# Performance work log

Hardware: AMD Instinct MI355X
Metric: run time of the kernel (lower is better)

The kernel has to match this reference:

```python
import jax, jax.numpy as jnp
import numpy as np

N, E, D = 50000, 800000, 128  # nodes, edges, n_feat


def setup_inputs() -> dict:
    key = jax.random.key(0)
    ks = jax.random.split(key, 12)
    scale = 1.0 / np.sqrt(D)

    def w(k):
        return jax.random.normal(k, (D, D), jnp.float32) * scale

    return {
        "h": jax.random.normal(ks[0], (N, D), jnp.float32),
        "src": jax.random.randint(ks[1], (E,), 0, N, jnp.int32),
        "dst": jax.random.randint(ks[2], (E,), 0, N, jnp.int32),
        # skip MLP: Linear -> ELU -> Linear
        "W_skip1": w(ks[3]), "b_skip1": jnp.zeros((D,), jnp.float32),
        "W_skip2": w(ks[4]), "b_skip2": jnp.zeros((D,), jnp.float32),
        # SAGEConv 1 (mean aggregator): fc_self, fc_neigh (bias-free) + shared bias
        "W_self1": w(ks[5]), "W_neigh1": w(ks[6]), "b_conv1": jnp.zeros((D,), jnp.float32),
        # self-interaction MLP
        "W_si1": w(ks[7]), "b_si1": jnp.zeros((D,), jnp.float32),
        "W_si2": w(ks[8]), "b_si2": jnp.zeros((D,), jnp.float32),
        # SAGEConv 2
        "W_self2": w(ks[9]), "W_neigh2": w(ks[10]), "b_conv2": jnp.zeros((D,), jnp.float32),
    }


def _sage_mean(h, src, dst, W_self, W_neigh, b):
    # DGL SAGEConv('mean'): fc_self(h) + fc_neigh(mean over in-neighbors of h_src) + bias
    n = h.shape[0]
    deg = jax.ops.segment_sum(jnp.ones((src.shape[0],), h.dtype), dst, num_segments=n)
    agg = jax.ops.segment_sum(h[src], dst, num_segments=n)  # [N, D] sum of neighbor feats
    agg = agg / jnp.maximum(deg, 1.0)[:, None]  # degree clamp for isolated nodes
    return h @ W_self + agg @ W_neigh + b


def reference(h, src, dst,
              W_skip1, b_skip1, W_skip2, b_skip2,
              W_self1, W_neigh1, b_conv1,
              W_si1, b_si1, W_si2, b_si2,
              W_self2, W_neigh2, b_conv2):
    elu = jax.nn.elu
    h_skip = elu(h @ W_skip1 + b_skip1) @ W_skip2 + b_skip2
    x = elu(_sage_mean(h, src, dst, W_self1, W_neigh1, b_conv1))
    x = elu(elu(x @ W_si1 + b_si1) @ W_si2 + b_si2)
    x = _sage_mean(x, src, dst, W_self2, W_neigh2, b_conv2)
    return h_skip + x
```

## Files before the change

kernel.cpp:

```cpp
#include <hip/hip_runtime.h>
#include <math.h>

#define NN 50000
#define NE 800000
#define NRT 782
#define NT  (NRT * 2)
#define NB  128
#define NPB2 391
#define EPB 2048
#define NBB 391

typedef __attribute__((ext_vector_type(8))) short short8;
typedef __attribute__((ext_vector_type(4))) float floatx4;

#define AS1 __attribute__((address_space(1)))
#define AS3 __attribute__((address_space(3)))

__device__ __forceinline__ unsigned short f2bf(float f) {
    unsigned u = __float_as_uint(f);
    unsigned r = (u + 0x7fff + ((u >> 16) & 1)) >> 16;
    return (unsigned short)r;
}
__device__ __forceinline__ float bf2f(unsigned short h) {
    return __uint_as_float(((unsigned)h) << 16);
}


__global__ __launch_bounds__(256)
void k_prep(const float* __restrict__ h, unsigned short* __restrict__ hB,
            const int* __restrict__ dst, int* __restrict__ bcnt,
            const float* w0, const float* w1, const float* w2, const float* w3,
            const float* w4, const float* w5, const float* w6, const float* w7,
            short* __restrict__ wpk) {
    int bid = blockIdx.x;
    const int t = threadIdx.x;
    if (bid < 3125) {
        int i = (bid * 256 + t) * 8;
        float4 a = *(const float4*)&h[i];
        float4 b = *(const float4*)&h[i + 4];
        short8 v;
        v[0] = (short)f2bf(a.x); v[1] = (short)f2bf(a.y);
        v[2] = (short)f2bf(a.z); v[3] = (short)f2bf(a.w);
        v[4] = (short)f2bf(b.x); v[5] = (short)f2bf(b.y);
        v[6] = (short)f2bf(b.z); v[7] = (short)f2bf(b.w);
        *(short8*)&hB[i] = v;
    } else if (bid < 3125 + NBB) {
        __shared__ int cnt[NB];
        if (t < NB) cnt[t] = 0;
        __syncthreads();
        int base = (bid - 3125) * EPB;
#pragma unroll
        for (int i = 0; i < 8; ++i) {
            int idx = base + i * 256 + t;
            if (idx < NE) atomicAdd(&cnt[dst[idx] / NPB2], 1);
        }
        __syncthreads();
        if (t < NB && cnt[t]) atomicAdd(&bcnt[t], cnt[t]);
    } else {
        int wb = bid - 3125 - NBB;
        const float* W;
        switch (wb) {
            case 0: W = w0; break; case 1: W = w1; break;
            case 2: W = w2; break; case 3: W = w3; break;
            case 4: W = w4; break; case 5: W = w5; break;
            case 6: W = w6; break; default: W = w7; break;
        }
        short* dstp = wpk + (size_t)wb * 16384;
#pragma unroll
        for (int i = 0; i < 8; ++i) {
            int q = t + i * 256;
            int cb = q >> 8, ks = (q >> 6) & 3, lane = q & 63;
            int n = lane & 15, g = lane >> 4;
            int col = cb * 16 + n, krow = ks * 32 + g * 8;
            short8 v;
#pragma unroll
            for (int j = 0; j < 8; ++j)
                v[j] = (short)f2bf(W[(krow + j) * 128 + col]);
            *(short8*)&dstp[q * 8] = v;
        }
    }
}


__global__ void k_bscan(const int* __restrict__ bcnt, int* __restrict__ gcur,
                        int* __restrict__ bstart) {
    __shared__ int s[NB];
    int t = threadIdx.x;
    int c = bcnt[t];
    s[t] = c;
    __syncthreads();
    for (int off = 1; off < NB; off <<= 1) {
        int v = (t >= off) ? s[t - off] : 0;
        __syncthreads();
        s[t] += v;
        __syncthreads();
    }
    int excl = s[t] - c;
    gcur[t] = excl;
    bstart[t] = excl;
    if (t == NB - 1) bstart[NB] = s[NB - 1];
}


__global__ __launch_bounds__(256)
void k_bucket(const int* __restrict__ src, const int* __restrict__ dst,
              int* __restrict__ gcur, int* __restrict__ bsrc, int* __restrict__ bdst) {
    __shared__ int psrc[EPB];
    __shared__ int pdst[EPB];
    __shared__ int cnt[NB];
    __shared__ int ebase[NB];
    __shared__ int gbase[NB];
    const int t = threadIdx.x;
    const int e0 = blockIdx.x * EPB;
    const int M = (e0 + EPB <= NE) ? EPB : (NE - e0);

    if (t < NB) cnt[t] = 0;
    __syncthreads();

    int es[8], ed[8], rank[8];
#pragma unroll
    for (int i = 0; i < 8; ++i) {
        int idx = i * 256 + t;
        if (idx < M) {
            es[i] = src[e0 + idx];
            ed[i] = dst[e0 + idx];
            rank[i] = atomicAdd(&cnt[ed[i] / NPB2], 1);
        }
    }
    __syncthreads();
    if (t < NB) ebase[t] = cnt[t];
    __syncthreads();
    for (int off = 1; off < NB; off <<= 1) {
        int v = 0;
        if (t < NB && t >= off) v = ebase[t - off];
        __syncthreads();
        if (t < NB) ebase[t] += v;
        __syncthreads();
    }
    if (t < NB) ebase[t] -= cnt[t];
    __syncthreads();
#pragma unroll
    for (int i = 0; i < 8; ++i) {
        int idx = i * 256 + t;
        if (idx < M) {
            int b = ed[i] / NPB2;
            int pos = ebase[b] + rank[i];
            psrc[pos] = es[i];
            pdst[pos] = ed[i];
        }
    }
    if (t < NB && cnt[t] > 0) gbase[t] = atomicAdd(&gcur[t], cnt[t]);
    __syncthreads();
#pragma unroll
    for (int i = 0; i < 8; ++i) {
        int idx = i * 256 + t;
        if (idx < M) {
            int d = pdst[idx];
            int b = d / NPB2;
            int gpos = gbase[b] + (idx - ebase[b]);
            bsrc[gpos] = psrc[idx];
            bdst[gpos] = d;
        }
    }
}


template<int DUAL, int DOELU, int OUTF32, int NOBIAS, int BIAS2>
__device__ __forceinline__ void gemm_body(
        int bid,
        const unsigned short* __restrict__ A, const unsigned short* __restrict__ A2,
        const short* __restrict__ Wp, const short* __restrict__ Wp2,
        const float* __restrict__ bias, const float* __restrict__ bias2,
        void* outv, short* sW, short* sA) {
    const int t = threadIdx.x;
    const int wv = t >> 6, lane = t & 63;
    const int rb = bid >> 1, ct = bid & 1;
    const int row0 = rb * 64, col0 = ct * 64;
    const int m = lane & 15, g = lane >> 4;

    floatx4 acc[4];
#pragma unroll
    for (int cb = 0; cb < 4; ++cb) acc[cb] = (floatx4){0.f, 0.f, 0.f, 0.f};

    const int npass = DUAL ? 2 : 1;
    for (int pass = 0; pass < npass; ++pass) {
        const unsigned short* Ac = pass ? A2 : A;
        const short* Wc = (pass ? Wp2 : Wp) + ct * 8192;
        __syncthreads();
#pragma unroll
        for (int i = 0; i < 4; ++i) {
            int cbase = (i * 4 + wv) * 64;
            __builtin_amdgcn_global_load_lds(
                (const AS1 unsigned int*)(Wc + (size_t)(cbase + lane) * 8),
                (AS3 unsigned int*)(sW + cbase * 8), 16, 0, 0);
        }
#pragma unroll
        for (int i = 0; i < 4; ++i) {
            int cbase = (i * 4 + wv) * 64;
            int id = cbase + lane;
            int r = id >> 4, cs = id & 15;
            int rg = row0 + r; if (rg >= NN) rg = NN - 1;
            int csrc = cs ^ (r & 7);
            __builtin_amdgcn_global_load_lds(
                (const AS1 unsigned int*)(Ac + (size_t)rg * 128 + csrc * 8),
                (AS3 unsigned int*)(sA + cbase * 8), 16, 0, 0);
        }
        asm volatile("s_waitcnt vmcnt(0)" ::: "memory");
        __builtin_amdgcn_sched_barrier(0);
        __syncthreads();

        const int r0 = wv * 16;
#pragma unroll
        for (int ks = 0; ks < 4; ++ks) {
            int cxor = (ks * 4 + g) ^ (m & 7);
            short8 af = *(const short8*)&sA[((r0 + m) * 16 + cxor) * 8];
#pragma unroll
            for (int cb = 0; cb < 4; ++cb) {
                short8 bf = *(const short8*)&sW[((cb * 4 + ks) * 64 + lane) * 8];
                acc[cb] = __builtin_amdgcn_mfma_f32_16x16x32_bf16(af, bf, acc[cb], 0, 0, 0);
            }
        }
    }

    const int rowbase = row0 + wv * 16 + g * 4;
#pragma unroll
    for (int cb = 0; cb < 4; ++cb) {
        int C = col0 + cb * 16 + m;
        float bb = NOBIAS ? 0.f : bias[C];
        if (BIAS2) bb += bias2[C];
#pragma unroll
        for (int rr = 0; rr < 4; ++rr) {
            int R = rowbase + rr;
            if (R < NN) {
                size_t idx = (size_t)R * 128 + C;
                float v = acc[cb][rr] + bb;
                if (DOELU) v = (v > 0.f) ? v : expm1f(v);
                if (OUTF32) ((float*)outv)[idx] = v;
                else        ((unsigned short*)outv)[idx] = f2bf(v);
            }
        }
    }
}

template<int DUAL, int DOELU, int OUTF32, int NOBIAS, int BIAS2>
__global__ __launch_bounds__(256)
void k_mm(const unsigned short* __restrict__ A, const unsigned short* __restrict__ A2,
          const short* __restrict__ Wp, const short* __restrict__ Wp2,
          const float* __restrict__ bias, const float* __restrict__ bias2,
          void* outv) {
    __shared__ short sMem[16384];
    gemm_body<DUAL, DOELU, OUTF32, NOBIAS, BIAS2>(blockIdx.x, A, A2, Wp, Wp2,
                                                  bias, bias2, outv, sMem, sMem + 8192);
}


__global__ __launch_bounds__(256)
void k_mega1(const int* __restrict__ bsrc, const int* __restrict__ bdst,
             const int* __restrict__ bstart, int* __restrict__ row_start,
             int* __restrict__ col_idx,
             const unsigned short* __restrict__ hB, const short* __restrict__ wpk,
             const float* __restrict__ bsk1,
             unsigned short* __restrict__ T1out, unsigned short* __restrict__ C1out,
             unsigned short* __restrict__ S1out) {
    __shared__ short sMem[16384];
    int bid = blockIdx.x;
    if (bid < NB) {
        int* lcur = (int*)sMem;
        int* sc   = lcur + NPB2;
        int* rs   = sc + 512;
        const int t = threadIdx.x;
        const int n0 = bid * NPB2;
        const int n1 = (n0 + NPB2 < NN) ? n0 + NPB2 : NN;
        const int nn = n1 - n0;
        const int w0 = bstart[bid], w1 = bstart[bid + 1];
        for (int i = t; i < nn; i += 256) lcur[i] = 0;
        __syncthreads();
        for (int e = w0 + t; e < w1; e += 256)
            atomicAdd(&lcur[bdst[e] - n0], 1);
        __syncthreads();
        int v0 = (t < nn) ? lcur[t] : 0;
        int v1 = (t + 256 < nn) ? lcur[t + 256] : 0;
        sc[t] = v0; sc[t + 256] = v1;
        __syncthreads();
        for (int off = 1; off < 512; off <<= 1) {
            int a0 = (t >= off) ? sc[t - off] : 0;
            int a1 = (t + 256 >= off) ? sc[t + 256 - off] : 0;
            __syncthreads();
            sc[t] += a0; sc[t + 256] += a1;
            __syncthreads();
        }
        for (int i = t; i < nn; i += 256) {
            int r = w0 + sc[i] - lcur[i];
            rs[i] = r;
            row_start[n0 + i] = r;
            lcur[i] = 0;
        }
        if (bid == 0 && t == 0) row_start[NN] = NE;
        __syncthreads();
        for (int e = w0 + t; e < w1; e += 256) {
            int d = bdst[e] - n0;
            int slot = atomicAdd(&lcur[d], 1);
            col_idx[rs[d] + slot] = bsrc[e];
        }
    } else if (bid < NB + NT) {
        gemm_body<0, 0, 0, 1, 0>(bid - NB, hB, nullptr, wpk + 3 * 16384, nullptr,
                                 nullptr, nullptr, T1out, sMem, sMem + 8192);
    } else if (bid < NB + 2 * NT) {
        gemm_body<0, 0, 0, 1, 0>(bid - NB - NT, hB, nullptr, wpk + 2 * 16384, nullptr,
                                 nullptr, nullptr, C1out, sMem, sMem + 8192);
    } else {
        gemm_body<0, 1, 0, 0, 0>(bid - NB - 2 * NT, hB, nullptr, wpk, nullptr,
                                 bsk1, nullptr, S1out, sMem, sMem + 8192);
    }
}


__global__ __launch_bounds__(256)
void k_agg1x(const unsigned short* __restrict__ T1, const int* __restrict__ row_start,
             const int* __restrict__ col_idx, const unsigned short* __restrict__ C1,
             const float* __restrict__ bc, unsigned short* __restrict__ X1out) {
    int node = (blockIdx.x * 256 + threadIdx.x) >> 6;
    int lane = threadIdx.x & 63;
    if (node >= NN) return;
    const int beg = row_start[node], end = row_start[node + 1];
    const size_t lo = (size_t)(lane * 2);
    float sx = 0.f, sy = 0.f;
    int j = beg;
#pragma unroll 1
    for (; j + 8 <= end; j += 8) {
        int s[8];
#pragma unroll
        for (int u = 0; u < 8; ++u) s[u] = col_idx[j + u];
        unsigned v[8];
#pragma unroll
        for (int u = 0; u < 8; ++u)
            v[u] = *(const unsigned*)&T1[(size_t)s[u] * 128 + lo];
#pragma unroll
        for (int u = 0; u < 8; ++u) {
            sx += bf2f((unsigned short)(v[u] & 0xffff));
            sy += bf2f((unsigned short)(v[u] >> 16));
        }
    }
#pragma unroll 1
    for (; j < end; ++j) {
        int s = col_idx[j];
        unsigned v = *(const unsigned*)&T1[(size_t)s * 128 + lo];
        sx += bf2f((unsigned short)(v & 0xffff));
        sy += bf2f((unsigned short)(v >> 16));
    }
    float inv = 1.0f / fmaxf((float)(end - beg), 1.0f);
    unsigned c = *(const unsigned*)&C1[(size_t)node * 128 + lo];
    float x = sx * inv + bf2f((unsigned short)(c & 0xffff)) + bc[lane * 2];
    float y = sy * inv + bf2f((unsigned short)(c >> 16)) + bc[lane * 2 + 1];
    x = (x > 0.f) ? x : expm1f(x);
    y = (y > 0.f) ? y : expm1f(y);
    unsigned o = (unsigned)f2bf(x) | ((unsigned)f2bf(y) << 16);
    *(unsigned*)&X1out[(size_t)node * 128 + lo] = o;
}


__global__ __launch_bounds__(256)
void k_mega3(const unsigned short* __restrict__ X3, const unsigned short* __restrict__ S1,
             const short* __restrict__ wpk, const float* __restrict__ bconv2,
             const float* __restrict__ bsk2, float* __restrict__ outP,
             unsigned short* __restrict__ T2out) {
    __shared__ short sMem[16384];
    int bid = blockIdx.x;
    if (bid < NT) {
        gemm_body<1, 0, 1, 0, 1>(bid, X3, S1, wpk + 6 * 16384, wpk + 1 * 16384,
                                 bconv2, bsk2, outP, sMem, sMem + 8192);
    } else {
        gemm_body<0, 0, 0, 1, 0>(bid - NT, X3, nullptr, wpk + 7 * 16384, nullptr,
                                 nullptr, nullptr, T2out, sMem, sMem + 8192);
    }
}


__global__ __launch_bounds__(256)
void k_aggf(const unsigned short* __restrict__ T2, const int* __restrict__ row_start,
            const int* __restrict__ col_idx, float* __restrict__ out) {
    int node = (blockIdx.x * 256 + threadIdx.x) >> 6;
    int lane = threadIdx.x & 63;
    if (node >= NN) return;
    const int beg = row_start[node], end = row_start[node + 1];
    const size_t lo = (size_t)(lane * 2);
    float sx = 0.f, sy = 0.f;
    int j = beg;
#pragma unroll 1
    for (; j + 8 <= end; j += 8) {
        int s[8];
#pragma unroll
        for (int u = 0; u < 8; ++u) s[u] = col_idx[j + u];
        unsigned v[8];
#pragma unroll
        for (int u = 0; u < 8; ++u)
            v[u] = *(const unsigned*)&T2[(size_t)s[u] * 128 + lo];
#pragma unroll
        for (int u = 0; u < 8; ++u) {
            sx += bf2f((unsigned short)(v[u] & 0xffff));
            sy += bf2f((unsigned short)(v[u] >> 16));
        }
    }
#pragma unroll 1
    for (; j < end; ++j) {
        int s = col_idx[j];
        unsigned v = *(const unsigned*)&T2[(size_t)s * 128 + lo];
        sx += bf2f((unsigned short)(v & 0xffff));
        sy += bf2f((unsigned short)(v >> 16));
    }
    float inv = 1.0f / fmaxf((float)(end - beg), 1.0f);
    float2* op = (float2*)&out[(size_t)node * 128 + lo];
    float2 v = *op;
    v.x += sx * inv;
    v.y += sy * inv;
    *op = v;
}


extern "C" void kernel_launch(void* const* d_in, const int* in_sizes, int n_in,
                              void* d_out, int out_size, void* d_ws, size_t ws_size,
                              hipStream_t stream) {
    const float* h        = (const float*)d_in[0];
    const int*   src      = (const int*)d_in[1];
    const int*   dst      = (const int*)d_in[2];
    const float* W_skip1  = (const float*)d_in[3];
    const float* b_skip1  = (const float*)d_in[4];
    const float* W_skip2  = (const float*)d_in[5];
    const float* b_skip2  = (const float*)d_in[6];
    const float* W_self1  = (const float*)d_in[7];
    const float* W_neigh1 = (const float*)d_in[8];
    const float* b_conv1  = (const float*)d_in[9];
    const float* W_si1    = (const float*)d_in[10];
    const float* b_si1    = (const float*)d_in[11];
    const float* W_si2    = (const float*)d_in[12];
    const float* b_si2    = (const float*)d_in[13];
    const float* W_self2  = (const float*)d_in[14];
    const float* W_neigh2 = (const float*)d_in[15];
    const float* b_conv2  = (const float*)d_in[16];
    float* out = (float*)d_out;

    char* ws = (char*)d_ws;
    int* bcnt      = (int*)ws;
    int* gcur      = bcnt + 128;
    int* bstart    = bcnt + 256;
    int* row_start = bcnt + 100096;
    int* col_idx   = bcnt + 150272;
    short* wpk          = (short*)(ws + 3801088);
    unsigned short* hB  = (unsigned short*)(ws + 4063232);
    unsigned short* B1  = (unsigned short*)(ws + 16863232);
    unsigned short* B2  = (unsigned short*)(ws + 29663232);
    int* bsrc           = (int*)(ws + 42463232);
    int* bdst           = (int*)(ws + 45663232);
    unsigned short* C1s = (unsigned short*)d_out;

    hipMemsetAsync(ws, 0, 128 * sizeof(int), stream);

    k_prep<<<3125 + NBB + 8, 256, 0, stream>>>(h, hB, dst, bcnt,
                                               W_skip1, W_skip2, W_self1, W_neigh1,
                                               W_si1, W_si2, W_self2, W_neigh2, wpk);
    k_bscan<<<1, NB, 0, stream>>>(bcnt, gcur, bstart);

    k_bucket<<<NBB, 256, 0, stream>>>(src, dst, gcur, bsrc, bdst);

    k_mega1<<<NB + 3 * NT, 256, 0, stream>>>(bsrc, bdst, bstart, row_start, col_idx,
                                             hB, wpk, b_skip1, B1, C1s, B2);

    k_agg1x<<<12500, 256, 0, stream>>>(B1, row_start, col_idx, C1s, b_conv1, hB);

    k_mm<0, 1, 0, 0, 0><<<NT, 256, 0, stream>>>(hB, nullptr, wpk + 4 * 16384, nullptr,
                                                b_si1, nullptr, B1);
    k_mm<0, 1, 0, 0, 0><<<NT, 256, 0, stream>>>(B1, nullptr, wpk + 5 * 16384, nullptr,
                                                b_si2, nullptr, hB);

    k_mega3<<<2 * NT, 256, 0, stream>>>(hB, B2, wpk, b_conv2, b_skip2, out, B1);

    k_aggf<<<12500, 256, 0, stream>>>(B1, row_start, col_idx, out);
}
```

Measured before the change: 199.5 us.

## Share A tile across three GEMMs and split gather over half-wavefronts

The three GEMMs in the first mega kernel that all read hB now run in one block, which loads the A tile into LDS once and then cycles through the three weight matrices. This replaces three separate block sets that each reloaded the same A rows. Separately, both aggregation kernels now split each wavefront into two halves that handle alternate edges with 8-byte loads, then combine the halves with a cross-lane shuffle. The gather is meant to keep more distinct rows in flight per instruction, at the cost of fewer blocks in the fused GEMM and one extra reduction step.

Result: faster. 189.2 us (-5.1%).

```diff
diff --git a/kernel.cpp b/kernel.cpp
--- a/kernel.cpp
+++ b/kernel.cpp
@@ -254,6 +254,84 @@
 }
 
 
+__device__ __forceinline__ void gemm3_body(
+        int bid, const unsigned short* __restrict__ A,
+        const short* __restrict__ Wn, const short* __restrict__ Ws,
+        const short* __restrict__ Wk, const float* __restrict__ bsk1,
+        unsigned short* __restrict__ T1, unsigned short* __restrict__ C1,
+        unsigned short* __restrict__ S1, short* sW, short* sA) {
+    const int t = threadIdx.x;
+    const int wv = t >> 6, lane = t & 63;
+    const int rb = bid >> 1, ct = bid & 1;
+    const int row0 = rb * 64, col0 = ct * 64;
+    const int m = lane & 15, g = lane >> 4;
+
+#pragma unroll
+    for (int i = 0; i < 4; ++i) {
+        int cbase = (i * 4 + wv) * 64;
+        int id = cbase + lane;
+        int r = id >> 4, cs = id & 15;
+        int rg = row0 + r; if (rg >= NN) rg = NN - 1;
+        int csrc = cs ^ (r & 7);
+        __builtin_amdgcn_global_load_lds(
+            (const AS1 unsigned int*)(A + (size_t)rg * 128 + csrc * 8),
+            (AS3 unsigned int*)(sA + cbase * 8), 16, 0, 0);
+    }
+
+#pragma unroll
+    for (int ph = 0; ph < 3; ++ph) {
+        if (ph) __syncthreads();
+        const short* Wc = (ph == 0 ? Wn : ph == 1 ? Ws : Wk) + ct * 8192;
+#pragma unroll
+        for (int i = 0; i < 4; ++i) {
+            int cbase = (i * 4 + wv) * 64;
+            __builtin_amdgcn_global_load_lds(
+                (const AS1 unsigned int*)(Wc + (size_t)(cbase + lane) * 8),
+                (AS3 unsigned int*)(sW + cbase * 8), 16, 0, 0);
+        }
+        asm volatile("s_waitcnt vmcnt(0)" ::: "memory");
+        __builtin_amdgcn_sched_barrier(0);
+        __syncthreads();
+
+        floatx4 acc[4];
+#pragma unroll
+        for (int cb = 0; cb < 4; ++cb) acc[cb] = (floatx4){0.f, 0.f, 0.f, 0.f};
+        const int r0 = wv * 16;
+#pragma unroll
+        for (int ks = 0; ks < 4; ++ks) {
+            int cxor = (ks * 4 + g) ^ (m & 7);
+            short8 af = *(const short8*)&sA[((r0 + m) * 16 + cxor) * 8];
+#pragma unroll
+            for (int cb = 0; cb < 4; ++cb) {
+                short8 bf = *(const short8*)&sW[((cb * 4 + ks) * 64 + lane) * 8];
+                acc[cb] = __builtin_amdgcn_mfma_f32_16x16x32_bf16(af, bf, acc[cb], 0, 0, 0);
+            }
+        }
+
+        const int rowbase = row0 + wv * 16 + g * 4;
+#pragma unroll
+        for (int cb = 0; cb < 4; ++cb) {
+            int C = col0 + cb * 16 + m;
+            float bb = (ph == 2) ? bsk1[C] : 0.f;
+#pragma unroll
+            for (int rr = 0; rr < 4; ++rr) {
+                int R = rowbase + rr;
+                if (R < NN) {
+                    size_t idx = (size_t)R * 128 + C;
+                    float v = acc[cb][rr] + bb;
+                    if (ph == 0)      T1[idx] = f2bf(v);
+                    else if (ph == 1) C1[idx] = f2bf(v);
+                    else {
+                        v = (v > 0.f) ? v : expm1f(v);
+                        S1[idx] = f2bf(v);
+                    }
+                }
+            }
+        }
+    }
+}
+
+
 __global__ __launch_bounds__(256)
 void k_mega1(const int* __restrict__ bsrc, const int* __restrict__ bdst,
              const int* __restrict__ bstart, int* __restrict__ row_start,
@@ -302,15 +380,9 @@
             int slot = atomicAdd(&lcur[d], 1);
             col_idx[rs[d] + slot] = bsrc[e];
         }
-    } else if (bid < NB + NT) {
-        gemm_body<0, 0, 0, 1, 0>(bid - NB, hB, nullptr, wpk + 3 * 16384, nullptr,
-                                 nullptr, nullptr, T1out, sMem, sMem + 8192);
-    } else if (bid < NB + 2 * NT) {
-        gemm_body<0, 0, 0, 1, 0>(bid - NB - NT, hB, nullptr, wpk + 2 * 16384, nullptr,
-                                 nullptr, nullptr, C1out, sMem, sMem + 8192);
     } else {
-        gemm_body<0, 1, 0, 0, 0>(bid - NB - 2 * NT, hB, nullptr, wpk, nullptr,
-                                 bsk1, nullptr, S1out, sMem, sMem + 8192);
+        gemm3_body(bid - NB, hB, wpk + 3 * 16384 , wpk + 2 * 16384 ,
+                   wpk , bsk1, T1out, C1out, S1out, sMem, sMem + 8192);
     }
 }
 
@@ -322,40 +394,61 @@
     int node = (blockIdx.x * 256 + threadIdx.x) >> 6;
     int lane = threadIdx.x & 63;
     if (node >= NN) return;
+    const int grp = lane >> 5, gl = lane & 31;
     const int beg = row_start[node], end = row_start[node + 1];
-    const size_t lo = (size_t)(lane * 2);
-    float sx = 0.f, sy = 0.f;
+    const size_t lo = (size_t)(gl * 4);
+    float a0 = 0.f, a1 = 0.f, a2 = 0.f, a3 = 0.f;
     int j = beg;
 #pragma unroll 1
     for (; j + 8 <= end; j += 8) {
-        int s[8];
-#pragma unroll
-        for (int u = 0; u < 8; ++u) s[u] = col_idx[j + u];
-        unsigned v[8];
-#pragma unroll
-        for (int u = 0; u < 8; ++u)
-            v[u] = *(const unsigned*)&T1[(size_t)s[u] * 128 + lo];
-#pragma unroll
-        for (int u = 0; u < 8; ++u) {
-            sx += bf2f((unsigned short)(v[u] & 0xffff));
-            sy += bf2f((unsigned short)(v[u] >> 16));
+        int s[4];
+#pragma unroll
+        for (int u = 0; u < 4; ++u) s[u] = col_idx[j + 2 * u + grp];
+        uint2 v[4];
+#pragma unroll
+        for (int u = 0; u < 4; ++u)
+            v[u] = *(const uint2*)&T1[(size_t)s[u] * 128 + lo];
+#pragma unroll
+        for (int u = 0; u < 4; ++u) {
+            a0 += bf2f((unsigned short)(v[u].x & 0xffff));
+            a1 += bf2f((unsigned short)(v[u].x >> 16));
+            a2 += bf2f((unsigned short)(v[u].y & 0xffff));
+            a3 += bf2f((unsigned short)(v[u].y >> 16));
         }
     }
 #pragma unroll 1
-    for (; j < end; ++j) {
-        int s = col_idx[j];
-        unsigned v = *(const unsigned*)&T1[(size_t)s * 128 + lo];
-        sx += bf2f((unsigned short)(v & 0xffff));
-        sy += bf2f((unsigned short)(v >> 16));
-    }
-    float inv = 1.0f / fmaxf((float)(end - beg), 1.0f);
-    unsigned c = *(const unsigned*)&C1[(size_t)node * 128 + lo];
-    float x = sx * inv + bf2f((unsigned short)(c & 0xffff)) + bc[lane * 2];
-    float y = sy * inv + bf2f((unsigned short)(c >> 16)) + bc[lane * 2 + 1];
-    x = (x > 0.f) ? x : expm1f(x);
-    y = (y > 0.f) ? y : expm1f(y);
-    unsigned o = (unsigned)f2bf(x) | ((unsigned)f2bf(y) << 16);
-    *(unsigned*)&X1out[(size_t)node * 128 + lo] = o;
+    for (; j < end; j += 2) {
+        int e = j + grp;
+        if (e < end) {
+            int s = col_idx[e];
+            uint2 v = *(const uint2*)&T1[(size_t)s * 128 + lo];
+            a0 += bf2f((unsigned short)(v.x & 0xffff));
+            a1 += bf2f((unsigned short)(v.x >> 16));
+            a2 += bf2f((unsigned short)(v.y & 0xffff));
+            a3 += bf2f((unsigned short)(v.y >> 16));
+        }
+    }
+    a0 += __shfl_xor(a0, 32);
+    a1 += __shfl_xor(a1, 32);
+    a2 += __shfl_xor(a2, 32);
+    a3 += __shfl_xor(a3, 32);
+    if (lane < 32) {
+        float inv = 1.0f / fmaxf((float)(end - beg), 1.0f);
+        uint2 c = *(const uint2*)&C1[(size_t)node * 128 + lo];
+        float4 bv = *(const float4*)&bc[lane * 4];
+        float x0 = a0 * inv + bf2f((unsigned short)(c.x & 0xffff)) + bv.x;
+        float x1 = a1 * inv + bf2f((unsigned short)(c.x >> 16)) + bv.y;
+        float x2 = a2 * inv + bf2f((unsigned short)(c.y & 0xffff)) + bv.z;
+        float x3 = a3 * inv + bf2f((unsigned short)(c.y >> 16)) + bv.w;
+        x0 = (x0 > 0.f) ? x0 : expm1f(x0);
+        x1 = (x1 > 0.f) ? x1 : expm1f(x1);
+        x2 = (x2 > 0.f) ? x2 : expm1f(x2);
+        x3 = (x3 > 0.f) ? x3 : expm1f(x3);
+        uint2 o;
+        o.x = (unsigned)f2bf(x0) | ((unsigned)f2bf(x1) << 16);
+        o.y = (unsigned)f2bf(x2) | ((unsigned)f2bf(x3) << 16);
+        *(uint2*)&X1out[(size_t)node * 128 + lo] = o;
+    }
 }
 
 
@@ -382,38 +475,52 @@
     int node = (blockIdx.x * 256 + threadIdx.x) >> 6;
     int lane = threadIdx.x & 63;
     if (node >= NN) return;
+    const int grp = lane >> 5, gl = lane & 31;
     const int beg = row_start[node], end = row_start[node + 1];
-    const size_t lo = (size_t)(lane * 2);
-    float sx = 0.f, sy = 0.f;
+    const size_t lo = (size_t)(gl * 4);
+    float a0 = 0.f, a1 = 0.f, a2 = 0.f, a3 = 0.f;
     int j = beg;
 #pragma unroll 1
     for (; j + 8 <= end; j += 8) {
-        int s[8];
-#pragma unroll
-        for (int u = 0; u < 8; ++u) s[u] = col_idx[j + u];
-        unsigned v[8];
-#pragma unroll
-        for (int u = 0; u < 8; ++u)
-            v[u] = *(const unsigned*)&T2[(size_t)s[u] * 128 + lo];
-#pragma unroll
-        for (int u = 0; u < 8; ++u) {
-            sx += bf2f((unsigned short)(v[u] & 0xffff));
-            sy += bf2f((unsigned short)(v[u] >> 16));
+        int s[4];
+#pragma unroll
+        for (int u = 0; u < 4; ++u) s[u] = col_idx[j + 2 * u + grp];
+        uint2 v[4];
+#pragma unroll
+        for (int u = 0; u < 4; ++u)
+            v[u] = *(const uint2*)&T2[(size_t)s[u] * 128 + lo];
+#pragma unroll
+        for (int u = 0; u < 4; ++u) {
+            a0 += bf2f((unsigned short)(v[u].x & 0xffff));
+            a1 += bf2f((unsigned short)(v[u].x >> 16));
+            a2 += bf2f((unsigned short)(v[u].y & 0xffff));
+            a3 += bf2f((unsigned short)(v[u].y >> 16));
         }
     }
 #pragma unroll 1
-    for (; j < end; ++j) {
-        int s = col_idx[j];
-        unsigned v = *(const unsigned*)&T2[(size_t)s * 128 + lo];
-        sx += bf2f((unsigned short)(v & 0xffff));
-        sy += bf2f((unsigned short)(v >> 16));
-    }
-    float inv = 1.0f / fmaxf((float)(end - beg), 1.0f);
-    float2* op = (float2*)&out[(size_t)node * 128 + lo];
-    float2 v = *op;
-    v.x += sx * inv;
-    v.y += sy * inv;
-    *op = v;
+    for (; j < end; j += 2) {
+        int e = j + grp;
+        if (e < end) {
+            int s = col_idx[e];
+            uint2 v = *(const uint2*)&T2[(size_t)s * 128 + lo];
+            a0 += bf2f((unsigned short)(v.x & 0xffff));
+            a1 += bf2f((unsigned short)(v.x >> 16));
+            a2 += bf2f((unsigned short)(v.y & 0xffff));
+            a3 += bf2f((unsigned short)(v.y >> 16));
+        }
+    }
+    a0 += __shfl_xor(a0, 32);
+    a1 += __shfl_xor(a1, 32);
+    a2 += __shfl_xor(a2, 32);
+    a3 += __shfl_xor(a3, 32);
+    if (lane < 32) {
+        float inv = 1.0f / fmaxf((float)(end - beg), 1.0f);
+        float4* op = (float4*)&out[(size_t)node * 128 + lo];
+        float4 v = *op;
+        v.x += a0 * inv; v.y += a1 * inv;
+        v.z += a2 * inv; v.w += a3 * inv;
+        *op = v;
+    }
 }
 
 
@@ -462,8 +569,8 @@
 
     k_bucket<<<NBB, 256, 0, stream>>>(src, dst, gcur, bsrc, bdst);
 
-    k_mega1<<<NB + 3 * NT, 256, 0, stream>>>(bsrc, bdst, bstart, row_start, col_idx,
-                                             hB, wpk, b_skip1, B1, C1s, B2);
+    k_mega1<<<NB + NT, 256, 0, stream>>>(bsrc, bdst, bstart, row_start, col_idx,
+                                         hB, wpk, b_skip1, B1, C1s, B2);
 
     k_agg1x<<<12500, 256, 0, stream>>>(B1, row_start, col_idx, C1s, b_conv1, hB);
 
```
